# Optimization experiments

Hardware: AMD Instinct MI355X
Metric: run time of the kernel (lower is better)

Reference implementation:

```python
import jax, jax.numpy as jnp
import numpy as np

B, H, W = 4, 192, 192
CIN, CB, CM = 64, 16, 256   # backbone out, bottleneck, mask channels
TOPK = 16
TEMP = 1.0
COLOR_NORM = 1.0
BN_EPS = 1e-5


def setup_inputs() -> dict:
    key = jax.random.key(0)
    k0, k1, k2, k3 = jax.random.split(key, 4)
    img = jax.random.uniform(k0, (B, 3, H, W), jnp.float32)
    base_feat = jax.random.normal(k1, (B, CIN, H, W), jnp.float32)
    w_bneck = jax.random.normal(k2, (CB, CIN), jnp.float32) * 0.05
    b_bneck = jnp.zeros((CB,), jnp.float32)
    bn_gamma = jnp.ones((CB,), jnp.float32)
    bn_beta = jnp.zeros((CB,), jnp.float32)
    w_mask = jax.random.normal(k3, (CM, CB), jnp.float32) * 0.05
    return dict(img=img, base_feat=base_feat, w_bneck=w_bneck, b_bneck=b_bneck,
                bn_gamma=bn_gamma, bn_beta=bn_beta, w_mask=w_mask, num_colors=256)


def reference(img, base_feat, w_bneck, b_bneck, bn_gamma, bn_beta, w_mask, num_colors):
    b, _, h, w = img.shape
    # bottleneck: 1x1 conv + BatchNorm (training batch stats) + ReLU
    x = jnp.einsum('bchw,oc->bohw', base_feat, w_bneck) + b_bneck[None, :, None, None]
    mean = x.mean(axis=(0, 2, 3))
    var = x.var(axis=(0, 2, 3))
    x = (x - mean[None, :, None, None]) * jax.lax.rsqrt(var + BN_EPS)[None, :, None, None]
    feat = jax.nn.relu(x * bn_gamma[None, :, None, None] + bn_beta[None, :, None, None])
    # color mask: 1x1 conv (no bias) -> [B, 256, H, W]
    m = jnp.einsum('bchw,oc->bohw', feat, w_mask)
    # fold 256 channels into num_colors groups and sum -> [B, K, H, W]
    m = m.reshape(b, -1, num_colors, h, w).sum(axis=1)
    k = min(TOPK, num_colors)
    # top-k over the color axis, softmax, scatter back into sparse mask
    mt = jnp.transpose(m, (0, 2, 3, 1))              # [B, H, W, K]
    vals, idx = jax.lax.top_k(mt, k)                 # [B, H, W, k]
    sm = jax.nn.softmax(vals / TEMP, axis=-1)
    m_sp = jnp.zeros_like(mt).at[
        jnp.arange(b)[:, None, None, None],
        jnp.arange(h)[None, :, None, None],
        jnp.arange(w)[None, None, :, None],
        idx].set(sm)
    m_sp = jnp.transpose(m_sp, (0, 3, 1, 2))         # [B, K, H, W]
    # weighted color palette: avoid the [B,3,K,H,W] intermediate via einsum
    num = jnp.einsum('bchw,bkhw->bck', img, m_sp)    # [B, 3, K]
    den = m_sp.sum(axis=(2, 3))[:, None, :] + 1e-8   # [B, 1, K]
    color_palette = num / den / COLOR_NORM           # [B, 3, K]
    transformed_img = jnp.einsum('bkhw,bck->bchw', m_sp, color_palette)
    return transformed_img, m_sp, color_palette[:, :, :, None, None]
```

## Files before the change

### kernel.cpp

```cpp
#include <hip/hip_runtime.h>

#define HW    36864
#define NB    4
#define NCH   256
#define CIN   64
#define CB    16
#define NPIX  (NB*HW)
#define DELTA 1e-4f

typedef short bf16x8 __attribute__((ext_vector_type(8)));
typedef float f32x4  __attribute__((ext_vector_type(4)));

struct FlagEntry {
  unsigned pix;
  unsigned char cnt, need, r0, r1;
  unsigned char ks[8];
};


__device__ __forceinline__ unsigned short bf16_rne(float x) {
  unsigned u = __float_as_uint(x);
  unsigned r = u + 0x7fffu + ((u >> 16) & 1u);
  return (unsigned short)(r >> 16);
}
__device__ __forceinline__ float bf16_tof(unsigned short h) {
  return __uint_as_float(((unsigned)h) << 16);
}


template<bool ASC>
__device__ __forceinline__ void bitonic16(float* v) {
  #pragma unroll
  for (int K = 2; K <= 16; K <<= 1) {
    #pragma unroll
    for (int J = K >> 1; J > 0; J >>= 1) {
      #pragma unroll
      for (int i = 0; i < 16; ++i) {
        int l = i ^ J;
        if (l > i) {
          bool up = (((i & K) == 0) == ASC);
          float a = v[i], b = v[l];
          float lo = fminf(a, b), hi = fmaxf(a, b);
          v[i] = up ? lo : hi;
          v[l] = up ? hi : lo;
        }
      }
    }
  }
}

__device__ __forceinline__ void bmerge16_desc(float* v) {
  #pragma unroll
  for (int J = 8; J > 0; J >>= 1) {
    #pragma unroll
    for (int i = 0; i < 16; ++i) {
      int l = i ^ J;
      if (l > i) {
        float a = v[i], b = v[l];
        float lo = fminf(a, b), hi = fmaxf(a, b);
        v[i] = hi; v[l] = lo;
      }
    }
  }
}


__global__ void k0_zero(unsigned* flagcnt) { *flagcnt = 0u; }


__global__ __launch_bounds__(256) void k1_conv(
    const float* __restrict__ bfeat, const float* __restrict__ wb,
    const float* __restrict__ bb, float* __restrict__ xout,
    double* __restrict__ part)
{
  __shared__ float wbT[CIN][CB];
  __shared__ double redS[4][CB];
  __shared__ double redQ[4][CB];
  const int t = threadIdx.x;
  for (int i = t; i < CIN*CB; i += 256) {
    int o = i >> 6, c = i & 63;
    wbT[c][o] = wb[i];
  }
  __syncthreads();

  const int blk = blockIdx.x;
  const int b = blk / 144, seg = blk % 144;
  const int p = seg * 256 + t;
  const float* bfb = bfeat + (size_t)b * CIN * HW;

  float acc[CB];
  #pragma unroll
  for (int o = 0; o < CB; ++o) acc[o] = bb[o];

  for (int c = 0; c < CIN; ++c) {
    float v = bfb[(size_t)c*HW + p];
    #pragma unroll
    for (int o4 = 0; o4 < 4; ++o4) {
      float4 w4 = *(const float4*)&wbT[c][o4*4];
      acc[o4*4+0] = fmaf(v, w4.x, acc[o4*4+0]);
      acc[o4*4+1] = fmaf(v, w4.y, acc[o4*4+1]);
      acc[o4*4+2] = fmaf(v, w4.z, acc[o4*4+2]);
      acc[o4*4+3] = fmaf(v, w4.w, acc[o4*4+3]);
    }
  }

  float* xb = xout + (size_t)b * CB * HW;
  #pragma unroll
  for (int o = 0; o < CB; ++o) xb[(size_t)o*HW + p] = acc[o];

  const int wv = t >> 6, lane = t & 63;
  #pragma unroll
  for (int o = 0; o < CB; ++o) {
    double a = (double)acc[o], q = a*a;
    for (int off = 32; off; off >>= 1) { a += __shfl_xor(a, off); q += __shfl_xor(q, off); }
    if (lane == 0) { redS[wv][o] = a; redQ[wv][o] = q; }
  }
  __syncthreads();
  if (t < CB) {
    double a = redS[0][t] + redS[1][t] + redS[2][t] + redS[3][t];
    part[(size_t)blk*32 + t] = a;
  } else if (t < 32) {
    int o = t - CB;
    double q = redQ[0][o] + redQ[1][o] + redQ[2][o] + redQ[3][o];
    part[(size_t)blk*32 + t] = q;
  }
}


__global__ __launch_bounds__(64) void k1b_stats(
    const double* __restrict__ part, const float* __restrict__ gam,
    const float* __restrict__ bet, double* __restrict__ st64, float* __restrict__ st32)
{
  __shared__ double sh[32];
  const int t = threadIdx.x;
  if (t < 32) {
    double a = 0.0;
    #pragma unroll 8
    for (int i = 0; i < 576; ++i) a += part[(size_t)i*32 + t];
    sh[t] = a;
  }
  __syncthreads();
  if (t < CB) {
    const double N = (double)NPIX;
    double mean = sh[t] / N;
    double var  = sh[16+t] / N - mean*mean;
    double rstd = 1.0 / sqrt(var + 1e-5);
    double scl = (double)gam[t] * rstd;
    double sft = (double)bet[t] - mean*scl;
    st64[t] = scl; st64[CB+t] = sft;
    st32[t] = (float)scl; st32[CB+t] = (float)sft;
  }
}


__global__ __launch_bounds__(256) void k1c_bfrag(
    const float* __restrict__ wm, short* __restrict__ bfrag)
{
  const int t = threadIdx.x;
  for (int e = t; e < 2048; e += 256) {
    const int v = e >> 10, ct = (e >> 6) & 15, l = e & 63;
    const int n = l & 15, g = l >> 4;
    const int col = ct*16 + n;
    short out[8];
    #pragma unroll
    for (int j = 0; j < 8; ++j) {
      const int k = g*8 + j;
      const int kk = k & 15;
      const bool hi_half = (k < 16);
      float w = wm[col*CB + kk];
      unsigned short hb = bf16_rne(w);
      float res = w - bf16_tof(hb);
      unsigned short lb = bf16_rne(res);
      bool use_hi = ((v == 0) == hi_half);
      out[j] = (short)(use_hi ? hb : lb);
    }
    bf16x8 pk;
    #pragma unroll
    for (int j = 0; j < 8; ++j) pk[j] = out[j];
    *(bf16x8*)&bfrag[(size_t)e * 8] = pk;
  }
}


__device__ __forceinline__ void k2_epilogue(int b, int p, int pxl,
    int selN, int nearN, int nselN,
    float* lcw, unsigned char* lidx, unsigned char* lnear,
    unsigned* cidx, float* cw, unsigned* flagcnt, FlagEntry* entries)
{
  int start = selN < 16 ? selN : 16;
  for (int j = start; j < 16; ++j) { lcw[pxl*16 + j] = 0.f; lidx[pxl*16 + j] = 0; }
  unsigned g = (unsigned)(b*HW + p);
  uint4 iv = *(uint4*)&lidx[pxl*16];
  ((uint4*)cidx)[g] = iv;
  float4* cwq = (float4*)cw;
  #pragma unroll
  for (int q = 0; q < 4; ++q) cwq[(size_t)g*4 + q] = *(float4*)&lcw[pxl*16 + q*4];
  bool flag = (nearN > 1) || (selN != 16);
  if (flag) {
    unsigned slot = atomicAdd(flagcnt, 1u);
    FlagEntry e;
    e.pix = g;
    int cnt = nearN < 8 ? nearN : 8;
    e.cnt = (unsigned char)cnt;
    int nsure = selN - nselN;
    int need = 16 - nsure;
    if (need < 0) need = 0;
    if (need > cnt) need = cnt;
    e.need = (unsigned char)need;
    e.r0 = (nearN > 8 || selN != 16) ? 1 : 0;
    e.r1 = 0;
    #pragma unroll
    for (int j = 0; j < 8; ++j) e.ks[j] = (j < cnt) ? lnear[pxl*8 + j] : 0;
    entries[slot] = e;
  }
}

#define MSTRIDE 260

__global__ __launch_bounds__(256, 2) void k2_main(
    const float* __restrict__ x, const short* __restrict__ bfrag,
    const float* __restrict__ st32, float* __restrict__ msp,
    unsigned* __restrict__ cidx, float* __restrict__ cw,
    unsigned* __restrict__ flagcnt, FlagEntry* __restrict__ entries)
{
  extern __shared__ char smem[];
  float* m_lds = (float*)smem;
  char* uni = smem + 64*MSTRIDE*4;
  float* lcw = (float*)uni;
  unsigned char* lidx  = (unsigned char*)(uni + 4096);
  unsigned char* lnear = (unsigned char*)(uni + 5120);
  short* A_st = (short*)uni;

  const int t = threadIdx.x;
  const int blk = blockIdx.x;
  const int b = blk / 576;
  const int p0 = (blk % 576) * 64;
  const float* xb = x + (size_t)b*CB*HW + p0;

  #pragma unroll
  for (int r = 0; r < 4; ++r) {
    int e = r*256 + t;
    int o = e >> 6, pl = e & 63;
    float vx = xb[(size_t)o*HW + pl];
    float f = fmaxf(0.f, fmaf(vx, st32[o], st32[CB+o]));
    unsigned short hb = bf16_rne(f);
    float res = f - bf16_tof(hb);
    unsigned short lb = bf16_rne(res);
    A_st[pl*40 + o]      = (short)hb;
    A_st[pl*40 + 16 + o] = (short)lb;
  }
  __syncthreads();

  const int w = t >> 6, l = t & 63;

  {
    const int prow = w*16 + (l & 15);
    const int k0 = (l >> 4) * 8;
    bf16x8 a = *(const bf16x8*)&A_st[prow*40 + k0];
    const int rowo = w*16 + (l >> 4)*4;
    const int coln = l & 15;
    #pragma unroll
    for (int ct = 0; ct < 16; ++ct) {
      bf16x8 b1 = *(const bf16x8*)&bfrag[(size_t)(ct*64 + l)*8];
      bf16x8 b2 = *(const bf16x8*)&bfrag[(size_t)((16 + ct)*64 + l)*8];
      f32x4 acc = {0.f, 0.f, 0.f, 0.f};
      acc = __builtin_amdgcn_mfma_f32_16x16x32_bf16(a, b1, acc, 0, 0, 0);
      acc = __builtin_amdgcn_mfma_f32_16x16x32_bf16(a, b2, acc, 0, 0, 0);
      #pragma unroll
      for (int i = 0; i < 4; ++i)
        m_lds[(rowo + i)*MSTRIDE + ct*16 + coln] = acc[i];
    }
  }
  __syncthreads();

  const int p = t >> 2, q = t & 3;
  float mv[64];
  #pragma unroll
  for (int r = 0; r < 16; ++r) {
    f32x4 v4 = *(const f32x4*)&m_lds[p*MSTRIDE + q*64 + r*4];
    mv[r*4+0] = v4[0]; mv[r*4+1] = v4[1]; mv[r*4+2] = v4[2]; mv[r*4+3] = v4[3];
  }

  float T[16], tmp[16];
  #pragma unroll
  for (int i = 0; i < 16; ++i) tmp[i] = mv[i];
  bitonic16<false>(tmp);
  #pragma unroll
  for (int i = 0; i < 16; ++i) T[i] = tmp[i];
  #pragma unroll
  for (int c = 1; c < 4; ++c) {
    #pragma unroll
    for (int i = 0; i < 16; ++i) tmp[i] = mv[c*16 + i];
    bitonic16<true>(tmp);
    #pragma unroll
    for (int i = 0; i < 16; ++i) T[i] = fmaxf(T[i], tmp[i]);
    bmerge16_desc(T);
  }
  {
    float R[16];
    #pragma unroll
    for (int i = 0; i < 16; ++i) R[i] = fmaxf(T[i], __shfl_xor(T[15-i], 1));
    bmerge16_desc(R);
    #pragma unroll
    for (int i = 0; i < 16; ++i) T[i] = R[i];
    #pragma unroll
    for (int i = 0; i < 16; ++i) R[i] = fmaxf(T[i], __shfl_xor(T[15-i], 2));
    bmerge16_desc(R);
    #pragma unroll
    for (int i = 0; i < 16; ++i) T[i] = R[i];
  }
  const float tau = T[15], top = T[0];
  float Z = 0.f;
  #pragma unroll
  for (int i = 0; i < 16; ++i) Z += __expf(T[i] - top);
  const float iZ = 1.f / Z;

  int cs = 0, cn = 0, cns = 0;
  #pragma unroll
  for (int j = 0; j < 64; ++j) {
    float v = mv[j];
    bool s = (v >= tau);
    bool nr = (fabsf(v - tau) <= DELTA);
    cs += s ? 1 : 0; cn += nr ? 1 : 0; cns += (s && nr) ? 1 : 0;
  }
  const int lb_ = l & ~3;
  int c0 = __shfl(cs, lb_), c1 = __shfl(cs, lb_+1), c2 = __shfl(cs, lb_+2), c3 = __shfl(cs, lb_+3);
  int n0 = __shfl(cn, lb_), n1 = __shfl(cn, lb_+1), n2 = __shfl(cn, lb_+2), n3 = __shfl(cn, lb_+3);
  int s0 = __shfl(cns, lb_), s1 = __shfl(cns, lb_+1), s2 = __shfl(cns, lb_+2), s3 = __shfl(cns, lb_+3);
  int offs = (q > 0 ? c0 : 0) + (q > 1 ? c1 : 0) + (q > 2 ? c2 : 0);
  int offn = (q > 0 ? n0 : 0) + (q > 1 ? n1 : 0) + (q > 2 ? n2 : 0);
  const int selN = c0 + c1 + c2 + c3;
  const int nearN = n0 + n1 + n2 + n3;
  const int nselN = s0 + s1 + s2 + s3;

  float* mspb = msp + (size_t)b*NCH*HW + p0;
  int isel = 0, inear = 0;
  #pragma unroll
  for (int j = 0; j < 64; ++j) {
    const int k = q*64 + j;
    float v = mv[j];
    bool s = (v >= tau);
    bool nr = (fabsf(v - tau) <= DELTA);
    float wv = s ? __expf(v - top) * iZ : 0.f;
    mspb[(size_t)k*HW + p] = wv;
    if (s) {
      int slot = offs + isel;
      if (slot < 16) { lcw[p*16 + slot] = wv; lidx[p*16 + slot] = (unsigned char)k; }
      ++isel;
    }
    if (nr) {
      int gs = offn + inear;
      if (gs < 8) lnear[p*8 + gs] = (unsigned char)k;
      ++inear;
    }
  }

  if (q == 0)
    k2_epilogue(b, p0 + p, p, selN, nearN, nselN, lcw, lidx, lnear,
                cidx, cw, flagcnt, entries);
}


__global__ __launch_bounds__(64) void k2b_fix(
    const float* __restrict__ bfeat, const float* __restrict__ wb,
    const float* __restrict__ bb, const float* __restrict__ wmg,
    const double* __restrict__ st64,
    const unsigned* __restrict__ flagcnt, const FlagEntry* __restrict__ entries,
    float* __restrict__ msp, unsigned* __restrict__ cidx, float* __restrict__ cw)
{
  __shared__ float wbT[CB][CIN];
  __shared__ float  wOrigL[16];
  __shared__ int    kOrigL[16];
  __shared__ float  wnL[8];
  __shared__ int    kL[8];
  __shared__ double tvL[16];
  __shared__ int    tiL[16];
  __shared__ float  wvL[16];

  const int lane = threadIdx.x;
  for (int i = lane; i < CB*CIN; i += 64) wbT[i >> 6][i & 63] = wb[i];
  __syncthreads();

  const unsigned n = *flagcnt;
  for (unsigned idx = blockIdx.x; idx < n; idx += gridDim.x) {
    FlagEntry e = entries[idx];
    const int b = (int)(e.pix / HW), p = (int)(e.pix % HW);

    const double v = (double)bfeat[(size_t)b*CIN*HW + (size_t)lane*HW + p];
    double ft[CB];
    #pragma unroll
    for (int o = 0; o < CB; ++o) {
      double s = v * (double)wbT[o][lane];
      #pragma unroll
      for (int off = 32; off; off >>= 1) s += __shfl_xor(s, off);
      s += (double)bb[o];
      ft[o] = fmax(0.0, s*st64[o] + st64[CB+o]);
    }

    float* mb = msp + (size_t)b*NCH*HW;
    unsigned char* cb_ = (unsigned char*)cidx + (size_t)e.pix*16;
    float* cwp = cw + (size_t)e.pix*16;

    if (e.r0) {
      double mm[4]; int kk4[4];
      #pragma unroll
      for (int u = 0; u < 4; ++u) {
        const int k = lane + 64*u; kk4[u] = k;
        const float* wr = wmg + k*CB;
        double a = 0.0;
        #pragma unroll
        for (int c = 0; c < CB; ++c) a = fma(ft[c], (double)wr[c], a);
        mm[u] = a;
      }
      for (int j = 0; j < 16; ++j) {
        double bm = mm[0]; int bk = kk4[0];
        #pragma unroll
        for (int u = 1; u < 4; ++u) {
          bool gt = (mm[u] > bm) || (mm[u] == bm && kk4[u] < bk);
          if (gt) { bm = mm[u]; bk = kk4[u]; }
        }
        #pragma unroll
        for (int off = 32; off; off >>= 1) {
          double om = __shfl_xor(bm, off);
          int ok = __shfl_xor(bk, off);
          bool gt = (om > bm) || (om == bm && ok < bk);
          if (gt) { bm = om; bk = ok; }
        }
        if (lane == 0) { tvL[j] = bm; tiL[j] = bk; }
        #pragma unroll
        for (int u = 0; u < 4; ++u) if (kk4[u] == bk) mm[u] = -1.0e300;
      }
      __syncthreads();
      const double top = tvL[0];
      double ej = (lane < 16) ? exp(tvL[lane] - top) : 0.0;
      double Z = ej;
      #pragma unroll
      for (int off = 32; off; off >>= 1) Z += __shfl_xor(Z, off);
      if (lane < 16) wvL[lane] = (float)(ej / Z);
      __syncthreads();
      int tiR[16]; float wvR[16];
      #pragma unroll
      for (int j = 0; j < 16; ++j) { tiR[j] = tiL[j]; wvR[j] = wvL[j]; }
      #pragma unroll
      for (int u = 0; u < 4; ++u) {
        const int k = lane + 64*u;
        float wv = 0.f;
        #pragma unroll
        for (int j = 0; j < 16; ++j) if (tiR[j] == k) wv = wvR[j];
        mb[(size_t)k*HW + p] = wv;
      }
      if (lane == 0) {
        unsigned used = 0; int on = 0;
        for (int it = 0; it < 16; ++it) {
          int bk = 1 << 20;
          #pragma unroll
          for (int j = 0; j < 16; ++j)
            if (!((used >> j) & 1u) && tiR[j] < bk) bk = tiR[j];
          if (bk >= (1 << 20)) break;
          float bw = 0.f;
          #pragma unroll
          for (int j = 0; j < 16; ++j)
            if (tiR[j] == bk) { bw = wvR[j]; used |= (1u << j); }
          if (bw != 0.f && on < 16) { cb_[on] = (unsigned char)bk; cwp[on] = bw; ++on; }
        }
        for (int j = on; j < 16; ++j) { cb_[j] = 0; cwp[j] = 0.f; }
      }
      __syncthreads();
      continue;
    }

    const int cnt = (e.cnt > 8) ? 8 : (int)e.cnt;
    int need = (int)e.need; if (need > cnt) need = cnt;

    if (lane < 16) { wOrigL[lane] = cwp[lane]; kOrigL[lane] = (int)cb_[lane]; }
    __syncthreads();

    const int myk = (lane < cnt) ? (int)e.ks[lane] : 0x7fffffff;
    double mj = 0.0;
    if (lane < cnt) {
      const float* wr = wmg + myk*CB;
      #pragma unroll
      for (int c = 0; c < CB; ++c) mj = fma(ft[c], (double)wr[c], mj);
    }
    float woldj = 0.f;
    if (lane < cnt) {
      #pragma unroll
      for (int q = 0; q < 16; ++q) {
        if (kOrigL[q] == myk && wOrigL[q] > 0.f) woldj = wOrigL[q];
      }
    }
    int rankj = 0;
    #pragma unroll
    for (int j2 = 0; j2 < 8; ++j2) {
      double m2 = __shfl(mj, j2);
      int k2v = __shfl(myk, j2);
      if (lane < cnt && j2 < cnt && j2 != lane) {
        bool gt = (m2 > mj) || (m2 == mj && k2v < myk);
        rankj += gt ? 1 : 0;
      }
    }
    float w2[8];
    #pragma unroll
    for (int j2 = 0; j2 < 8; ++j2) w2[j2] = __shfl(woldj, j2);
    int nw = 0;
    #pragma unroll
    for (int j2 = 0; j2 < 8; ++j2) if (j2 < cnt && w2[j2] > 0.f) ++nw;
    float wnj = 0.f;
    if (lane < cnt && rankj < need && rankj < nw) {
      #pragma unroll
      for (int cand = 0; cand < 8; ++cand) {
        if (cand < cnt && w2[cand] > 0.f) {
          float xv = w2[cand];
          int cgt = 0, cge = 0;
          #pragma unroll
          for (int j2 = 0; j2 < 8; ++j2)
            if (j2 < cnt && w2[j2] > 0.f) { cgt += (w2[j2] > xv); cge += (w2[j2] >= xv); }
          if (cgt <= rankj && rankj < cge) wnj = xv;
        }
      }
    }
    if (lane < cnt) mb[(size_t)myk*HW + p] = wnj;
    if (lane < 8)  { wnL[lane] = wnj; kL[lane] = myk; }
    __syncthreads();

    if (lane == 0) {
      int on = 0, ii = 0, jj = 0;
      while (ii < 16 || jj < cnt) {
        if (ii < 16 && wOrigL[ii] <= 0.f) { ++ii; continue; }
        int ko = (ii < 16) ? kOrigL[ii] : (1 << 20);
        int kj = (jj < cnt) ? kL[jj] : (1 << 20);
        if (ko >= (1 << 20) && kj >= (1 << 20)) break;
        if (ko < kj) {
          if (on < 16) { cb_[on] = (unsigned char)ko; cwp[on] = wOrigL[ii]; ++on; }
          ++ii;
        } else if (kj < ko) {
          if (wnL[jj] > 0.f && on < 16) { cb_[on] = (unsigned char)kj; cwp[on] = wnL[jj]; ++on; }
          ++jj;
        } else {
          if (wnL[jj] > 0.f && on < 16) { cb_[on] = (unsigned char)kj; cwp[on] = wnL[jj]; ++on; }
          ++ii; ++jj;
        }
      }
      for (int j = on; j < 16; ++j) { cb_[j] = 0; cwp[j] = 0.f; }
    }
    __syncthreads();
  }
}


__global__ __launch_bounds__(256) void k3_accum(
    const uint4* __restrict__ cidx, const float4* __restrict__ cw4,
    const float* __restrict__ img, float* __restrict__ part)
{
  __shared__ float acc[1024];
  const int t = threadIdx.x, blk = blockIdx.x;
  for (int i = t; i < 1024; i += 256) acc[i] = 0.f;
  __syncthreads();
  const int b = blk / 144;
  const int p = (blk % 144) * 256 + t;
  const float* imb = img + (size_t)b*3*HW;
  const int g = b*HW + p;
  uint4 iv = cidx[g];
  unsigned ivq[4] = {iv.x, iv.y, iv.z, iv.w};
  float r = imb[p], g_ = imb[HW + p], bl = imb[2*HW + p];
  #pragma unroll
  for (int q = 0; q < 4; ++q) {
    float4 wv = cw4[(size_t)g*4 + q];
    float wvv[4] = {wv.x, wv.y, wv.z, wv.w};
    #pragma unroll
    for (int u = 0; u < 4; ++u) {
      int k = (int)((ivq[q] >> (8*u)) & 255u);
      float wgt = wvv[u];
      atomicAdd(&acc[k],       wgt * r);
      atomicAdd(&acc[256 + k], wgt * g_);
      atomicAdd(&acc[512 + k], wgt * bl);
      atomicAdd(&acc[768 + k], wgt);
    }
  }
  __syncthreads();
  for (int i = t; i < 1024; i += 256) part[(size_t)blk*1024 + i] = acc[i];
}


__global__ __launch_bounds__(256) void k4_pal(
    const float* __restrict__ part, float* __restrict__ out_pal)
{
  __shared__ float acc[1024];
  const int b = blockIdx.x, t = threadIdx.x;
  for (int s = t; s < 1024; s += 256) {
    float a = 0.f;
    for (int i = 0; i < 144; ++i) a += part[(size_t)(b*144 + i)*1024 + s];
    acc[s] = a;
  }
  __syncthreads();
  for (int s = t; s < 768; s += 256) {
    int k = s & 255;
    float den = acc[768 + k] + 1e-8f;
    out_pal[(size_t)b*768 + s] = acc[s] / den;
  }
}


__global__ __launch_bounds__(256) void k5_img(
    const uint4* __restrict__ cidx, const float4* __restrict__ cw4,
    const float* __restrict__ pal, float* __restrict__ outimg)
{
  __shared__ float lp[768];
  const int t = threadIdx.x, blk = blockIdx.x;
  const int b = blk / 144;
  for (int i = t; i < 768; i += 256) lp[i] = pal[(size_t)b*768 + i];
  __syncthreads();
  const int p = (blk % 144) * 256 + t;
  const int g = b*HW + p;
  uint4 iv = cidx[g];
  unsigned ivq[4] = {iv.x, iv.y, iv.z, iv.w};
  float r = 0.f, g_ = 0.f, bl = 0.f;
  #pragma unroll
  for (int q = 0; q < 4; ++q) {
    float4 wv = cw4[(size_t)g*4 + q];
    float wvv[4] = {wv.x, wv.y, wv.z, wv.w};
    #pragma unroll
    for (int u = 0; u < 4; ++u) {
      int k = (int)((ivq[q] >> (8*u)) & 255u);
      float wgt = wvv[u];
      r  = fmaf(wgt, lp[k],       r);
      g_ = fmaf(wgt, lp[256 + k], g_);
      bl = fmaf(wgt, lp[512 + k], bl);
    }
  }
  float* ob = outimg + (size_t)b*3*HW;
  ob[p] = r; ob[HW + p] = g_; ob[2*HW + p] = bl;
}


extern "C" void kernel_launch(void* const* d_in, const int* in_sizes, int n_in,
                              void* d_out, int out_size, void* d_ws, size_t ws_size,
                              hipStream_t stream)
{
  const float* img   = (const float*)d_in[0];
  const float* bfeat = (const float*)d_in[1];
  const float* wb    = (const float*)d_in[2];
  const float* bb    = (const float*)d_in[3];
  const float* gam   = (const float*)d_in[4];
  const float* bet   = (const float*)d_in[5];
  const float* wm    = (const float*)d_in[6];

  float* out_img = (float*)d_out;
  float* out_msp = (float*)d_out + 442368;
  float* out_pal = (float*)d_out + 38191104;

  char* w = (char*)d_ws;
  float*     ws_x       = (float*)(w);
  double*    ws_part    = (double*)(w + 9437184);
  double*    ws_st64    = (double*)(w + 9584640);
  float*     ws_st32    = (float*)(w + 9584896);
  unsigned*  ws_flagcnt = (unsigned*)(w + 9585152);
  FlagEntry* ws_entries = (FlagEntry*)(w + 9585408);
  unsigned*  ws_cidx    = (unsigned*)(w + 11944704);
  float*     ws_cw      = (float*)(w + 14304000);
  float*     ws_nd      = ws_x;
  short*     ws_bfrag   = (short*)(w + 23741184);

  k0_zero<<<dim3(1), dim3(1), 0, stream>>>(ws_flagcnt);
  k1_conv<<<dim3(576), dim3(256), 0, stream>>>(bfeat, wb, bb, ws_x, ws_part);
  k1b_stats<<<dim3(1), dim3(64), 0, stream>>>(ws_part, gam, bet, ws_st64, ws_st32);
  k1c_bfrag<<<dim3(1), dim3(256), 0, stream>>>(wm, ws_bfrag);
  k2_main<<<dim3(2304), dim3(256), 72192, stream>>>(ws_x, ws_bfrag, ws_st32, out_msp,
                                                    ws_cidx, ws_cw, ws_flagcnt, ws_entries);
  k2b_fix<<<dim3(4096), dim3(64), 0, stream>>>(bfeat, wb, bb, wm, ws_st64,
                                               ws_flagcnt, ws_entries, out_msp, ws_cidx, ws_cw);
  k3_accum<<<dim3(576), dim3(256), 0, stream>>>((const uint4*)ws_cidx, (const float4*)ws_cw,
                                                img, ws_nd);
  k4_pal<<<dim3(4), dim3(256), 0, stream>>>(ws_nd, out_pal);
  k5_img<<<dim3(576), dim3(256), 0, stream>>>((const uint4*)ws_cidx, (const float4*)ws_cw,
                                              out_pal, out_img);
}
```

Baseline: 295.9 us.

## Halve k2_main pixel tile to 32 and split channels over 8 lanes per pixel

The main mask/top-k kernel now processes 32 pixels per block instead of 64, halving LDS use and raising launch bounds to 4 blocks per CU. Each pixel's 256 channels are now split across 8 lanes of 32 values, cutting per-thread register arrays and adding a third cross-lane merge round. The MFMA work is redistributed so wave pairs share row tiles and split the column tiles, and LDS reads are rotated to reduce bank conflicts. The trade-off is more blocks, extra shuffle merges, and the same write pattern done at half the pixel width per block.

```diff
diff --git a/kernel.cpp b/kernel.cpp
--- a/kernel.cpp
+++ b/kernel.cpp
@@ -216,8 +216,9 @@
 }
 
 #define MSTRIDE 260
-
-__global__ __launch_bounds__(256, 2) void k2_main(
+#define PXB 32
+
+__global__ __launch_bounds__(256, 4) void k2_main(
     const float* __restrict__ x, const short* __restrict__ bfrag,
     const float* __restrict__ st32, float* __restrict__ msp,
     unsigned* __restrict__ cidx, float* __restrict__ cw,
@@ -225,22 +226,22 @@
 {
   extern __shared__ char smem[];
   float* m_lds = (float*)smem;
-  char* uni = smem + 64*MSTRIDE*4;
+  char* uni = smem + PXB*MSTRIDE*4;
   float* lcw = (float*)uni;
-  unsigned char* lidx  = (unsigned char*)(uni + 4096);
-  unsigned char* lnear = (unsigned char*)(uni + 5120);
+  unsigned char* lidx  = (unsigned char*)(uni + 2048);
+  unsigned char* lnear = (unsigned char*)(uni + 2560);
   short* A_st = (short*)uni;
 
   const int t = threadIdx.x;
   const int blk = blockIdx.x;
-  const int b = blk / 576;
-  const int p0 = (blk % 576) * 64;
+  const int b = blk / 1152;
+  const int p0 = (blk % 1152) * PXB;
   const float* xb = x + (size_t)b*CB*HW + p0;
 
   #pragma unroll
-  for (int r = 0; r < 4; ++r) {
+  for (int r = 0; r < 2; ++r) {
     int e = r*256 + t;
-    int o = e >> 6, pl = e & 63;
+    int o = e >> 5, pl = e & 31;
     float vx = xb[(size_t)o*HW + pl];
     float f = fmaxf(0.f, fmaf(vx, st32[o], st32[CB+o]));
     unsigned short hb = bf16_rne(f);
@@ -254,13 +255,15 @@
   const int w = t >> 6, l = t & 63;
 
   {
-    const int prow = w*16 + (l & 15);
+    const int rt = w & 1, ch = w >> 1;
+    const int prow = rt*16 + (l & 15);
     const int k0 = (l >> 4) * 8;
     bf16x8 a = *(const bf16x8*)&A_st[prow*40 + k0];
-    const int rowo = w*16 + (l >> 4)*4;
+    const int rowo = rt*16 + (l >> 4)*4;
     const int coln = l & 15;
     #pragma unroll
-    for (int ct = 0; ct < 16; ++ct) {
+    for (int cc = 0; cc < 8; ++cc) {
+      const int ct = ch*8 + cc;
       bf16x8 b1 = *(const bf16x8*)&bfrag[(size_t)(ct*64 + l)*8];
       bf16x8 b2 = *(const bf16x8*)&bfrag[(size_t)((16 + ct)*64 + l)*8];
       f32x4 acc = {0.f, 0.f, 0.f, 0.f};
@@ -273,12 +276,13 @@
   }
   __syncthreads();
 
-  const int p = t >> 2, q = t & 3;
-  float mv[64];
-  #pragma unroll
-  for (int r = 0; r < 16; ++r) {
-    f32x4 v4 = *(const f32x4*)&m_lds[p*MSTRIDE + q*64 + r*4];
-    mv[r*4+0] = v4[0]; mv[r*4+1] = v4[1]; mv[r*4+2] = v4[2]; mv[r*4+3] = v4[3];
+  const int p = t >> 3, q = t & 7;
+  float mv[32];
+  #pragma unroll
+  for (int r = 0; r < 8; ++r) {
+    const int c = (r + q) & 7;
+    f32x4 v4 = *(const f32x4*)&m_lds[p*MSTRIDE + q*32 + c*4];
+    mv[c*4+0] = v4[0]; mv[c*4+1] = v4[1]; mv[c*4+2] = v4[2]; mv[c*4+3] = v4[3];
   }
 
   float T[16], tmp[16];
@@ -288,23 +292,16 @@
   #pragma unroll
   for (int i = 0; i < 16; ++i) T[i] = tmp[i];
   #pragma unroll
-  for (int c = 1; c < 4; ++c) {
-    #pragma unroll
-    for (int i = 0; i < 16; ++i) tmp[i] = mv[c*16 + i];
-    bitonic16<true>(tmp);
-    #pragma unroll
-    for (int i = 0; i < 16; ++i) T[i] = fmaxf(T[i], tmp[i]);
-    bmerge16_desc(T);
-  }
-  {
+  for (int i = 0; i < 16; ++i) tmp[i] = mv[16 + i];
+  bitonic16<true>(tmp);
+  #pragma unroll
+  for (int i = 0; i < 16; ++i) T[i] = fmaxf(T[i], tmp[i]);
+  bmerge16_desc(T);
+  #pragma unroll
+  for (int mk = 1; mk <= 4; mk <<= 1) {
     float R[16];
     #pragma unroll
-    for (int i = 0; i < 16; ++i) R[i] = fmaxf(T[i], __shfl_xor(T[15-i], 1));
-    bmerge16_desc(R);
-    #pragma unroll
-    for (int i = 0; i < 16; ++i) T[i] = R[i];
-    #pragma unroll
-    for (int i = 0; i < 16; ++i) R[i] = fmaxf(T[i], __shfl_xor(T[15-i], 2));
+    for (int i = 0; i < 16; ++i) R[i] = fmaxf(T[i], __shfl_xor(T[15-i], mk));
     bmerge16_desc(R);
     #pragma unroll
     for (int i = 0; i < 16; ++i) T[i] = R[i];
@@ -317,27 +314,28 @@
 
   int cs = 0, cn = 0, cns = 0;
   #pragma unroll
-  for (int j = 0; j < 64; ++j) {
+  for (int j = 0; j < 32; ++j) {
     float v = mv[j];
     bool s = (v >= tau);
     bool nr = (fabsf(v - tau) <= DELTA);
     cs += s ? 1 : 0; cn += nr ? 1 : 0; cns += (s && nr) ? 1 : 0;
   }
-  const int lb_ = l & ~3;
-  int c0 = __shfl(cs, lb_), c1 = __shfl(cs, lb_+1), c2 = __shfl(cs, lb_+2), c3 = __shfl(cs, lb_+3);
-  int n0 = __shfl(cn, lb_), n1 = __shfl(cn, lb_+1), n2 = __shfl(cn, lb_+2), n3 = __shfl(cn, lb_+3);
-  int s0 = __shfl(cns, lb_), s1 = __shfl(cns, lb_+1), s2 = __shfl(cns, lb_+2), s3 = __shfl(cns, lb_+3);
-  int offs = (q > 0 ? c0 : 0) + (q > 1 ? c1 : 0) + (q > 2 ? c2 : 0);
-  int offn = (q > 0 ? n0 : 0) + (q > 1 ? n1 : 0) + (q > 2 ? n2 : 0);
-  const int selN = c0 + c1 + c2 + c3;
-  const int nearN = n0 + n1 + n2 + n3;
-  const int nselN = s0 + s1 + s2 + s3;
+  const int lb_ = l & ~7;
+  int offs = 0, offn = 0, selN = 0, nearN = 0, nselN = 0;
+  #pragma unroll
+  for (int j2 = 0; j2 < 8; ++j2) {
+    int cv = __shfl(cs, lb_ + j2);
+    int nv = __shfl(cn, lb_ + j2);
+    int sv = __shfl(cns, lb_ + j2);
+    selN += cv; nearN += nv; nselN += sv;
+    if (j2 < q) { offs += cv; offn += nv; }
+  }
 
   float* mspb = msp + (size_t)b*NCH*HW + p0;
   int isel = 0, inear = 0;
   #pragma unroll
-  for (int j = 0; j < 64; ++j) {
-    const int k = q*64 + j;
+  for (int j = 0; j < 32; ++j) {
+    const int k = q*32 + j;
     float v = mv[j];
     bool s = (v >= tau);
     bool nr = (fabsf(v - tau) <= DELTA);
@@ -665,7 +663,7 @@
   k1_conv<<<dim3(576), dim3(256), 0, stream>>>(bfeat, wb, bb, ws_x, ws_part);
   k1b_stats<<<dim3(1), dim3(64), 0, stream>>>(ws_part, gam, bet, ws_st64, ws_st32);
   k1c_bfrag<<<dim3(1), dim3(256), 0, stream>>>(wm, ws_bfrag);
-  k2_main<<<dim3(2304), dim3(256), 72192, stream>>>(ws_x, ws_bfrag, ws_st32, out_msp,
+  k2_main<<<dim3(4608), dim3(256), 36096, stream>>>(ws_x, ws_bfrag, ws_st32, out_msp,
                                                     ws_cidx, ws_cw, ws_flagcnt, ws_entries);
   k2b_fix<<<dim3(4096), dim3(64), 0, stream>>>(bfeat, wb, bb, wm, ws_st64,
                                                ws_flagcnt, ws_entries, out_msp, ws_cidx, ws_cw);
```

After: 314.2 us. 6.2% more time.

## Keep MFMA outputs in registers for top-k, drop LDS round-trip

Applied to the files above, without the earlier changes.

The mask matmul swaps the MFMA operands so that each lane's accumulator holds channel values for its own pixel. The top-k selection can then run directly on registers instead of staging a 64x256 float tile in LDS and reading it back. This removes about 66KB of dynamic shared memory and a barrier, and launch bounds rise to 3 blocks per CU for more occupancy. The lane-group shuffles are rearranged to match the new lane-to-channel mapping. The k2b_fix merge loop is also rewritten as a filter-then-append, which no longer keeps output entries sorted by channel index and risks register spills at 64 values per thread.

```diff
diff --git a/kernel.cpp b/kernel.cpp
--- a/kernel.cpp
+++ b/kernel.cpp
@@ -215,26 +215,24 @@
   }
 }
 
-#define MSTRIDE 260
-
-__global__ __launch_bounds__(256, 2) void k2_main(
+#define PXW 16
+#define PXB 64
+
+__global__ __launch_bounds__(256, 3) void k2_main(
     const float* __restrict__ x, const short* __restrict__ bfrag,
     const float* __restrict__ st32, float* __restrict__ msp,
     unsigned* __restrict__ cidx, float* __restrict__ cw,
     unsigned* __restrict__ flagcnt, FlagEntry* __restrict__ entries)
 {
-  extern __shared__ char smem[];
-  float* m_lds = (float*)smem;
-  char* uni = smem + 64*MSTRIDE*4;
-  float* lcw = (float*)uni;
-  unsigned char* lidx  = (unsigned char*)(uni + 4096);
-  unsigned char* lnear = (unsigned char*)(uni + 5120);
-  short* A_st = (short*)uni;
+  __shared__ short A_st[PXB*40];
+  __shared__ float lcw[PXB*16];
+  __shared__ __align__(16) unsigned char lidx[PXB*16];
+  __shared__ unsigned char lnear[PXB*8];
 
   const int t = threadIdx.x;
   const int blk = blockIdx.x;
   const int b = blk / 576;
-  const int p0 = (blk % 576) * 64;
+  const int p0 = (blk % 576) * PXB;
   const float* xb = x + (size_t)b*CB*HW + p0;
 
   #pragma unroll
@@ -252,33 +250,22 @@
   __syncthreads();
 
   const int w = t >> 6, l = t & 63;
-
-  {
-    const int prow = w*16 + (l & 15);
-    const int k0 = (l >> 4) * 8;
-    bf16x8 a = *(const bf16x8*)&A_st[prow*40 + k0];
-    const int rowo = w*16 + (l >> 4)*4;
-    const int coln = l & 15;
-    #pragma unroll
-    for (int ct = 0; ct < 16; ++ct) {
-      bf16x8 b1 = *(const bf16x8*)&bfrag[(size_t)(ct*64 + l)*8];
-      bf16x8 b2 = *(const bf16x8*)&bfrag[(size_t)((16 + ct)*64 + l)*8];
-      f32x4 acc = {0.f, 0.f, 0.f, 0.f};
-      acc = __builtin_amdgcn_mfma_f32_16x16x32_bf16(a, b1, acc, 0, 0, 0);
-      acc = __builtin_amdgcn_mfma_f32_16x16x32_bf16(a, b2, acc, 0, 0, 0);
-      #pragma unroll
-      for (int i = 0; i < 4; ++i)
-        m_lds[(rowo + i)*MSTRIDE + ct*16 + coln] = acc[i];
-    }
-  }
-  __syncthreads();
-
-  const int p = t >> 2, q = t & 3;
+  const int pl15 = l & 15;
+  const int q = l >> 4;
+  const int px = w*PXW + pl15;
+  const int p = p0 + px;
+
+  bf16x8 a = *(const bf16x8*)&A_st[px*40 + q*8];
   float mv[64];
   #pragma unroll
-  for (int r = 0; r < 16; ++r) {
-    f32x4 v4 = *(const f32x4*)&m_lds[p*MSTRIDE + q*64 + r*4];
-    mv[r*4+0] = v4[0]; mv[r*4+1] = v4[1]; mv[r*4+2] = v4[2]; mv[r*4+3] = v4[3];
+  for (int ct = 0; ct < 16; ++ct) {
+    bf16x8 b1 = *(const bf16x8*)&bfrag[(size_t)(ct*64 + l)*8];
+    bf16x8 b2 = *(const bf16x8*)&bfrag[(size_t)((16 + ct)*64 + l)*8];
+    f32x4 acc = {0.f, 0.f, 0.f, 0.f};
+    acc = __builtin_amdgcn_mfma_f32_16x16x32_bf16(b1, a, acc, 0, 0, 0);
+    acc = __builtin_amdgcn_mfma_f32_16x16x32_bf16(b2, a, acc, 0, 0, 0);
+    mv[ct*4+0] = acc[0]; mv[ct*4+1] = acc[1];
+    mv[ct*4+2] = acc[2]; mv[ct*4+3] = acc[3];
   }
 
   float T[16], tmp[16];
@@ -296,15 +283,11 @@
     for (int i = 0; i < 16; ++i) T[i] = fmaxf(T[i], tmp[i]);
     bmerge16_desc(T);
   }
-  {
+  #pragma unroll
+  for (int mk = 16; mk <= 32; mk <<= 1) {
     float R[16];
     #pragma unroll
-    for (int i = 0; i < 16; ++i) R[i] = fmaxf(T[i], __shfl_xor(T[15-i], 1));
-    bmerge16_desc(R);
-    #pragma unroll
-    for (int i = 0; i < 16; ++i) T[i] = R[i];
-    #pragma unroll
-    for (int i = 0; i < 16; ++i) R[i] = fmaxf(T[i], __shfl_xor(T[15-i], 2));
+    for (int i = 0; i < 16; ++i) R[i] = fmaxf(T[i], __shfl_xor(T[15-i], mk));
     bmerge16_desc(R);
     #pragma unroll
     for (int i = 0; i < 16; ++i) T[i] = R[i];
@@ -323,40 +306,43 @@
     bool nr = (fabsf(v - tau) <= DELTA);
     cs += s ? 1 : 0; cn += nr ? 1 : 0; cns += (s && nr) ? 1 : 0;
   }
-  const int lb_ = l & ~3;
-  int c0 = __shfl(cs, lb_), c1 = __shfl(cs, lb_+1), c2 = __shfl(cs, lb_+2), c3 = __shfl(cs, lb_+3);
-  int n0 = __shfl(cn, lb_), n1 = __shfl(cn, lb_+1), n2 = __shfl(cn, lb_+2), n3 = __shfl(cn, lb_+3);
-  int s0 = __shfl(cns, lb_), s1 = __shfl(cns, lb_+1), s2 = __shfl(cns, lb_+2), s3 = __shfl(cns, lb_+3);
-  int offs = (q > 0 ? c0 : 0) + (q > 1 ? c1 : 0) + (q > 2 ? c2 : 0);
-  int offn = (q > 0 ? n0 : 0) + (q > 1 ? n1 : 0) + (q > 2 ? n2 : 0);
-  const int selN = c0 + c1 + c2 + c3;
-  const int nearN = n0 + n1 + n2 + n3;
-  const int nselN = s0 + s1 + s2 + s3;
-
-  float* mspb = msp + (size_t)b*NCH*HW + p0;
+  int offs = 0, offn = 0, selN = 0, nearN = 0, nselN = 0;
+  #pragma unroll
+  for (int q2 = 0; q2 < 4; ++q2) {
+    int cv = __shfl(cs,  pl15 + 16*q2);
+    int nv = __shfl(cn,  pl15 + 16*q2);
+    int sv = __shfl(cns, pl15 + 16*q2);
+    selN += cv; nearN += nv; nselN += sv;
+    if (q2 < q) { offs += cv; offn += nv; }
+  }
+
+  float* mspb = msp + (size_t)b*NCH*HW;
   int isel = 0, inear = 0;
   #pragma unroll
-  for (int j = 0; j < 64; ++j) {
-    const int k = q*64 + j;
-    float v = mv[j];
-    bool s = (v >= tau);
-    bool nr = (fabsf(v - tau) <= DELTA);
-    float wv = s ? __expf(v - top) * iZ : 0.f;
-    mspb[(size_t)k*HW + p] = wv;
-    if (s) {
-      int slot = offs + isel;
-      if (slot < 16) { lcw[p*16 + slot] = wv; lidx[p*16 + slot] = (unsigned char)k; }
-      ++isel;
-    }
-    if (nr) {
-      int gs = offn + inear;
-      if (gs < 8) lnear[p*8 + gs] = (unsigned char)k;
-      ++inear;
+  for (int ct = 0; ct < 16; ++ct) {
+    #pragma unroll
+    for (int i = 0; i < 4; ++i) {
+      const int k = ct*16 + q*4 + i;
+      const float v = mv[ct*4+i];
+      const bool s = (v >= tau);
+      const bool nr = (fabsf(v - tau) <= DELTA);
+      float wv = s ? __expf(v - top) * iZ : 0.f;
+      mspb[(size_t)k*HW + p] = wv;
+      if (s) {
+        int slot = offs + isel;
+        if (slot < 16) { lcw[px*16 + slot] = wv; lidx[px*16 + slot] = (unsigned char)k; }
+        ++isel;
+      }
+      if (nr) {
+        int gs = offn + inear;
+        if (gs < 8) lnear[px*8 + gs] = (unsigned char)k;
+        ++inear;
+      }
     }
   }
 
   if (q == 0)
-    k2_epilogue(b, p0 + p, p, selN, nearN, nselN, lcw, lidx, lnear,
+    k2_epilogue(b, p, px, selN, nearN, nselN, lcw, lidx, lnear,
                 cidx, cw, flagcnt, entries);
 }
 
@@ -524,23 +510,23 @@
     __syncthreads();
 
     if (lane == 0) {
-      int on = 0, ii = 0, jj = 0;
-      while (ii < 16 || jj < cnt) {
-        if (ii < 16 && wOrigL[ii] <= 0.f) { ++ii; continue; }
-        int ko = (ii < 16) ? kOrigL[ii] : (1 << 20);
-        int kj = (jj < cnt) ? kL[jj] : (1 << 20);
-        if (ko >= (1 << 20) && kj >= (1 << 20)) break;
-        if (ko < kj) {
-          if (on < 16) { cb_[on] = (unsigned char)ko; cwp[on] = wOrigL[ii]; ++on; }
-          ++ii;
-        } else if (kj < ko) {
-          if (wnL[jj] > 0.f && on < 16) { cb_[on] = (unsigned char)kj; cwp[on] = wnL[jj]; ++on; }
-          ++jj;
-        } else {
-          if (wnL[jj] > 0.f && on < 16) { cb_[on] = (unsigned char)kj; cwp[on] = wnL[jj]; ++on; }
-          ++ii; ++jj;
+      unsigned char nk[16]; float nwv[16];
+      int on = 0;
+      for (int j = 0; j < 16; ++j) {
+        int ko = kOrigL[j]; float wo = wOrigL[j];
+        if (wo <= 0.f) continue;
+        bool isNear = false;
+        #pragma unroll
+        for (int j2 = 0; j2 < 8; ++j2)
+          if (j2 < cnt && kL[j2] == ko) isNear = true;
+        if (isNear) continue;
+        if (on < 16) { nk[on] = (unsigned char)ko; nwv[on] = wo; ++on; }
+      }
+      for (int j2 = 0; j2 < 8; ++j2)
+        if (j2 < cnt && wnL[j2] > 0.f && on < 16) {
+          nk[on] = (unsigned char)kL[j2]; nwv[on] = wnL[j2]; ++on;
         }
-      }
+      for (int j = 0; j < on; ++j) { cb_[j] = nk[j]; cwp[j] = nwv[j]; }
       for (int j = on; j < 16; ++j) { cb_[j] = 0; cwp[j] = 0.f; }
     }
     __syncthreads();
@@ -665,8 +651,8 @@
   k1_conv<<<dim3(576), dim3(256), 0, stream>>>(bfeat, wb, bb, ws_x, ws_part);
   k1b_stats<<<dim3(1), dim3(64), 0, stream>>>(ws_part, gam, bet, ws_st64, ws_st32);
   k1c_bfrag<<<dim3(1), dim3(256), 0, stream>>>(wm, ws_bfrag);
-  k2_main<<<dim3(2304), dim3(256), 72192, stream>>>(ws_x, ws_bfrag, ws_st32, out_msp,
-                                                    ws_cidx, ws_cw, ws_flagcnt, ws_entries);
+  k2_main<<<dim3(2304), dim3(256), 0, stream>>>(ws_x, ws_bfrag, ws_st32, out_msp,
+                                                ws_cidx, ws_cw, ws_flagcnt, ws_entries);
   k2b_fix<<<dim3(4096), dim3(64), 0, stream>>>(bfeat, wb, bb, wm, ws_st64,
                                                ws_flagcnt, ws_entries, out_msp, ws_cidx, ws_cw);
   k3_accum<<<dim3(576), dim3(256), 0, stream>>>((const uint4*)ws_cidx, (const float4*)ws_cw,
```

New measurement: 297.5 us. No clear change (+0.5%).
